# Kernel optimization log

Hardware: AMD Instinct MI355X
Metric: run time of the kernel (lower is better)

## Reference

```python
import jax, jax.numpy as jnp
import numpy as np

B, S, IDIM, D, T, DUR_MAX = 32, 512, 256, 256, 4096, 16
EPS = 1e-6
SIGMA_C = 2.0
PAD = 0
LOG_SQRT_2PI = 0.9189385332046727  # 0.5*log(2*pi)


def setup_inputs() -> dict:
    rng = np.random.default_rng(0)
    # durations in [1, DUR_MAX); clip so each row's total length <= T (ragged tails)
    durs = rng.integers(1, DUR_MAX, size=(B, S))
    excl = np.cumsum(durs, axis=-1) - durs
    durs = np.minimum(durs, np.maximum(T - excl, 0))
    # token ids in [1, IDIM) so PAD=0 only appears via explicit padding
    text = rng.integers(1, IDIM, size=(B, S))
    embed = rng.standard_normal((IDIM, D)).astype(np.float32)
    embed[PAD] = 0.0  # padding_idx=0 row is zeros in nn.Embedding
    return {
        "text": jnp.asarray(text, dtype=jnp.int64),
        "durs": jnp.asarray(durs, dtype=jnp.int64),
        "embed": jnp.asarray(embed),
        "total_time": T,
    }


def reference(text, durs, embed, total_time):
    # F.pad(text/durs, [0, 2]) with value 0
    text_p = jnp.pad(text, ((0, 0), (0, 2)), constant_values=PAD)   # [B, S+2]
    durs_p = jnp.pad(durs, ((0, 0), (0, 2)), constant_values=0)     # [B, S+2]
    S2 = text_p.shape[-1]

    cum = jnp.cumsum(durs_p, axis=-1)                               # [B, S+2]
    durs_f = durs_p.astype(jnp.float32)
    # token centers: durs/2 + exclusive cumsum
    c = durs_f / 2.0 + (cum - durs_p).astype(jnp.float32)           # [B, S+2]
    sig = durs_f / SIGMA_C + EPS                                    # [B, S+2]

    t = jnp.arange(total_time, dtype=jnp.float32) + 0.5             # [T]
    z = (t[None, :, None] - c[:, None, :]) / sig[:, None, :]        # [B, T, S+2]
    # Normal(c, sig).log_prob(t).exp()
    w = jnp.exp(-0.5 * z * z - jnp.log(sig)[:, None, :] - LOG_SQRT_2PI)

    # zero weights on pad tokens, then normalize over tokens
    token_pad = (text_p == PAD)                                     # [B, S+2]
    w = jnp.where(token_pad[:, None, :], 0.0, w)
    w = w / (w.sum(-1, keepdims=True) + EPS)

    # frames beyond a row's total duration correspond to pad in `repeats`:
    # zero all weights there, then set the last token column to 1.0
    time_invalid = jnp.arange(total_time)[None, :] >= cum[:, -1:]   # [B, T]
    w = jnp.where(time_invalid[:, :, None], 0.0, w)
    last_col = (jnp.arange(S2) == S2 - 1)
    w = jnp.where(time_invalid[:, :, None] & last_col[None, None, :], 1.0, w)

    emb = embed[text_p]                                             # [B, S+2, D]
    return jnp.einsum("bts,bsd->btd", w, emb)                       # [B, T, D]
```

## Files before the change

kernel.cpp:

```cpp
#include <hip/hip_runtime.h>

#define B_ 32
#define S_ 512
#define D_ 256
#define T_ 4096
#define IDIM_ 256
#define EPS_ 1e-6f
#define INV_SQRT_2PI 0.3989422804014327f
#define NHALF_LOG2E -0.7213475204444817f
#define W_ 32

typedef float float4n __attribute__((ext_vector_type(4)));

__global__ __launch_bounds__(512) void GaussianEmbedding_prep(
    const int* __restrict__ text, const int* __restrict__ durs,
    float4* __restrict__ toks, int* __restrict__ tof, int* __restrict__ totb)
{
    int b = blockIdx.x;
    int s = threadIdx.x;
    int dur = durs[b * S_ + s];
    int lane = s & 63, wv = s >> 6;

    int incl = dur;
    #pragma unroll
    for (int o = 1; o < 64; o <<= 1) {
        int v = __shfl_up(incl, o);
        if (lane >= o) incl += v;
    }
    __shared__ int wsum[8];
    __shared__ int stot;
    if (lane == 63) wsum[wv] = incl;
    __syncthreads();
    int woff = 0;
    for (int i = 0; i < wv; ++i) woff += wsum[i];
    int excl = woff + incl - dur;

    if (s == 0) {
        int tot = 0;
        for (int i = 0; i < 8; ++i) tot += wsum[i];
        totb[b] = tot;
        stot = tot;
    }
    __syncthreads();
    int total = stot;

    float df = (float)dur;
    float sig = df * 0.5f + EPS_;
    float inv = 1.0f / sig;
    float4 tk;
    tk.x = df * 0.5f + (float)excl;
    tk.y = inv;
    tk.z = INV_SQRT_2PI * inv;
    tk.w = __int_as_float(text[b * S_ + s] & (IDIM_ - 1));
    toks[b * S_ + s] = tk;

    for (int f = excl; f < excl + dur; ++f)
        tof[b * T_ + f] = s;
    for (int f = total + s; f < T_; f += S_)
        tof[b * T_ + f] = S_ - 1;
}

__global__ __launch_bounds__(256) void GaussianEmbedding_main(
    const float4n* __restrict__ toks, const int* __restrict__ tof,
    const int* __restrict__ totb, const float4n* __restrict__ embed4,
    float4n* __restrict__ out)
{
    int lane = threadIdx.x & 63;
    int wave = __builtin_amdgcn_readfirstlane(blockIdx.x * 4 + (threadIdx.x >> 6));
    int b  = wave >> 10;
    int t0 = (wave & 1023) * 4;

    int total = totb[b];

    float4n a0 = {0,0,0,0}, a1 = {0,0,0,0}, a2 = {0,0,0,0}, a3 = {0,0,0,0};

    if (t0 < total) {
        int tlo = t0 - W_;      if (tlo < 0) tlo = 0;
        int thi = t0 + 3 + W_;  if (thi > total - 1) thi = total - 1;
        int lo = tof[b * T_ + tlo];
        int hi = tof[b * T_ + thi];
        if (lo < 0) lo = 0; if (hi > S_ - 1) hi = S_ - 1; if (hi < lo) hi = lo;
        lo = __builtin_amdgcn_readfirstlane(lo);
        hi = __builtin_amdgcn_readfirstlane(hi);

        float c0 = (float)t0 + 0.5f, c1 = c0 + 1.f, c2 = c0 + 2.f, c3 = c0 + 3.f;
        float p0 = 0.f, p1 = 0.f, p2 = 0.f, p3 = 0.f;
        #pragma unroll 2
        for (int s = lo; s <= hi; ++s) {
            float4n tk = toks[b * S_ + s];
            int tok = __float_as_int(tk.w);
            float4n ev = embed4[tok * (D_ / 4) + lane];
            float z0 = (c0 - tk.x) * tk.y;
            float z1 = (c1 - tk.x) * tk.y;
            float z2 = (c2 - tk.x) * tk.y;
            float z3 = (c3 - tk.x) * tk.y;
            float w0 = exp2f(NHALF_LOG2E * z0 * z0) * tk.z;
            float w1 = exp2f(NHALF_LOG2E * z1 * z1) * tk.z;
            float w2 = exp2f(NHALF_LOG2E * z2 * z2) * tk.z;
            float w3 = exp2f(NHALF_LOG2E * z3 * z3) * tk.z;
            p0 += w0; p1 += w1; p2 += w2; p3 += w3;
            a0 += w0 * ev; a1 += w1 * ev; a2 += w2 * ev; a3 += w3 * ev;
        }
        float s0 = (t0 + 0 < total) ? 1.0f / (p0 + EPS_) : 0.0f;
        float s1 = (t0 + 1 < total) ? 1.0f / (p1 + EPS_) : 0.0f;
        float s2 = (t0 + 2 < total) ? 1.0f / (p2 + EPS_) : 0.0f;
        float s3 = (t0 + 3 < total) ? 1.0f / (p3 + EPS_) : 0.0f;
        a0 *= s0; a1 *= s1; a2 *= s2; a3 *= s3;
    }

    size_t base = (size_t)(b * T_ + t0) * (D_ / 4) + lane;
    __builtin_nontemporal_store(a0, out + base);
    __builtin_nontemporal_store(a1, out + base + (D_ / 4));
    __builtin_nontemporal_store(a2, out + base + 2 * (D_ / 4));
    __builtin_nontemporal_store(a3, out + base + 3 * (D_ / 4));
}

extern "C" void kernel_launch(void* const* d_in, const int* in_sizes, int n_in,
                              void* d_out, int out_size, void* d_ws, size_t ws_size,
                              hipStream_t stream)
{
    const int* text    = (const int*)d_in[0];
    const int* durs    = (const int*)d_in[1];
    const float* embed = (const float*)d_in[2];

    float4* toks = (float4*)d_ws;
    int* tof  = (int*)((char*)d_ws + (size_t)B_ * S_ * sizeof(float4));
    int* totb = tof + (size_t)B_ * T_;

    GaussianEmbedding_prep<<<B_, S_, 0, stream>>>(text, durs, toks, tof, totb);
    GaussianEmbedding_main<<<(B_ * T_) / 16, 256, 0, stream>>>(
        (const float4n*)toks, tof, totb, (const float4n*)embed, (float4n*)d_out);
}
```

Before: 158.8 us.

## Compute Gaussian weights lane-parallel and process eight frames per wave

```diff
diff --git a/kernel.cpp b/kernel.cpp
--- a/kernel.cpp
+++ b/kernel.cpp
@@ -8,7 +8,8 @@
 #define EPS_ 1e-6f
 #define INV_SQRT_2PI 0.3989422804014327f
 #define NHALF_LOG2E -0.7213475204444817f
-#define W_ 32
+#define W_ 28
+#define FPW_ 8
 
 typedef float float4n __attribute__((ext_vector_type(4)));
 
@@ -67,52 +68,74 @@
 {
     int lane = threadIdx.x & 63;
     int wave = __builtin_amdgcn_readfirstlane(blockIdx.x * 4 + (threadIdx.x >> 6));
-    int b  = wave >> 10;
-    int t0 = (wave & 1023) * 4;
+    int b  = wave >> 9;
+    int t0 = (wave & 511) * FPW_;
 
     int total = totb[b];
 
-    float4n a0 = {0,0,0,0}, a1 = {0,0,0,0}, a2 = {0,0,0,0}, a3 = {0,0,0,0};
+    float4n acc[FPW_];
+    #pragma unroll
+    for (int f = 0; f < FPW_; ++f) acc[f] = (float4n){0.f, 0.f, 0.f, 0.f};
 
     if (t0 < total) {
-        int tlo = t0 - W_;      if (tlo < 0) tlo = 0;
-        int thi = t0 + 3 + W_;  if (thi > total - 1) thi = total - 1;
+        int tlo = t0 - W_;              if (tlo < 0) tlo = 0;
+        int thi = t0 + FPW_ - 1 + W_;   if (thi > total - 1) thi = total - 1;
         int lo = tof[b * T_ + tlo];
         int hi = tof[b * T_ + thi];
         if (lo < 0) lo = 0; if (hi > S_ - 1) hi = S_ - 1; if (hi < lo) hi = lo;
         lo = __builtin_amdgcn_readfirstlane(lo);
         hi = __builtin_amdgcn_readfirstlane(hi);
+        int nrel = hi - lo;
 
-        float c0 = (float)t0 + 0.5f, c1 = c0 + 1.f, c2 = c0 + 2.f, c3 = c0 + 3.f;
-        float p0 = 0.f, p1 = 0.f, p2 = 0.f, p3 = 0.f;
-        #pragma unroll 2
-        for (int s = lo; s <= hi; ++s) {
-            float4n tk = toks[b * S_ + s];
-            int tok = __float_as_int(tk.w);
-            float4n ev = embed4[tok * (D_ / 4) + lane];
-            float z0 = (c0 - tk.x) * tk.y;
-            float z1 = (c1 - tk.x) * tk.y;
-            float z2 = (c2 - tk.x) * tk.y;
-            float z3 = (c3 - tk.x) * tk.y;
-            float w0 = exp2f(NHALF_LOG2E * z0 * z0) * tk.z;
-            float w1 = exp2f(NHALF_LOG2E * z1 * z1) * tk.z;
-            float w2 = exp2f(NHALF_LOG2E * z2 * z2) * tk.z;
-            float w3 = exp2f(NHALF_LOG2E * z3 * z3) * tk.z;
-            p0 += w0; p1 += w1; p2 += w2; p3 += w3;
-            a0 += w0 * ev; a1 += w1 * ev; a2 += w2 * ev; a3 += w3 * ev;
+        int fl = lane >> 3;
+        int j0 = lane & 7;
+        float tcf = (float)(t0 + fl) + 0.5f;
+        float pacc = 0.f;
+
+        for (int chunk = 0; chunk <= nrel; chunk += 8) {
+            int idx = chunk + j0;
+            int cidx = idx > nrel ? nrel : idx;
+            float4n tk = toks[b * S_ + lo + cidx];
+            float z = (tcf - tk.x) * tk.y;
+            float w = exp2f(NHALF_LOG2E * z * z) * tk.z;
+            if (idx > nrel) w = 0.f;
+
+            float ws = w;
+            ws += __shfl_xor(ws, 1);
+            ws += __shfl_xor(ws, 2);
+            ws += __shfl_xor(ws, 4);
+            pacc += ws;
+
+            int wbits = __float_as_int(w);
+            int tbits = __float_as_int(tk.w);
+            #pragma unroll
+            for (int j = 0; j < 8; ++j) {
+                if (chunk + j <= nrel) {
+                    int tok = __builtin_amdgcn_readlane(tbits, j);
+                    float4n ev = embed4[tok * (D_ / 4) + lane];
+                    #pragma unroll
+                    for (int f = 0; f < FPW_; ++f) {
+                        float wf = __int_as_float(
+                            __builtin_amdgcn_readlane(wbits, f * 8 + j));
+                        acc[f] += wf * ev;
+                    }
+                }
+            }
         }
-        float s0 = (t0 + 0 < total) ? 1.0f / (p0 + EPS_) : 0.0f;
-        float s1 = (t0 + 1 < total) ? 1.0f / (p1 + EPS_) : 0.0f;
-        float s2 = (t0 + 2 < total) ? 1.0f / (p2 + EPS_) : 0.0f;
-        float s3 = (t0 + 3 < total) ? 1.0f / (p3 + EPS_) : 0.0f;
-        a0 *= s0; a1 *= s1; a2 *= s2; a3 *= s3;
+
+        int pbits = __float_as_int(pacc);
+        #pragma unroll
+        for (int f = 0; f < FPW_; ++f) {
+            float pf = __int_as_float(__builtin_amdgcn_readlane(pbits, f * 8));
+            float sf = (t0 + f < total) ? 1.0f / (pf + EPS_) : 0.0f;
+            acc[f] *= sf;
+        }
     }
 
     size_t base = (size_t)(b * T_ + t0) * (D_ / 4) + lane;
-    __builtin_nontemporal_store(a0, out + base);
-    __builtin_nontemporal_store(a1, out + base + (D_ / 4));
-    __builtin_nontemporal_store(a2, out + base + 2 * (D_ / 4));
-    __builtin_nontemporal_store(a3, out + base + 3 * (D_ / 4));
+    #pragma unroll
+    for (int f = 0; f < FPW_; ++f)
+        __builtin_nontemporal_store(acc[f], out + base + (size_t)f * (D_ / 4));
 }
 
 extern "C" void kernel_launch(void* const* d_in, const int* in_sizes, int n_in,
@@ -128,6 +151,6 @@
     int* totb = tof + (size_t)B_ * T_;
 
     GaussianEmbedding_prep<<<B_, S_, 0, stream>>>(text, durs, toks, tof, totb);
-    GaussianEmbedding_main<<<(B_ * T_) / 16, 256, 0, stream>>>(
+    GaussianEmbedding_main<<<(B_ * T_) / (FPW_ * 4), 256, 0, stream>>>(
         (const float4n*)toks, tof, totb, (const float4n*)embed, (float4n*)d_out);
 }
```

New measurement: 153.0 us. -3.7%, faster.
